# Kernel tuning notes

Hardware: AMD Instinct MI355X
Metric: run time of the kernel (lower is better)

The kernel has to match this reference:

```python
import jax, jax.numpy as jnp
import numpy as np

# Fixed multi-scale geometry implied by the module's hard-coded reshapes
# (48^2=2304, 24^2=576, 12^2=144; Len_q = 576).
SPATIAL = [(48, 48), (24, 24), (12, 12)]
NH, NP, NL = 6, 4, 3  # num_heads, num_points, num_levels


def _process_reference_points(rp):
    """rp: (B, 3024, 2) normalized refs over 3 levels -> (B, 576, 2).
    Mirrors the part1/part2/part3 averaging in MSDeformAttn.forward."""
    B = rp.shape[0]
    p1 = rp[:, :2304].reshape(B, 48, 48, 2).mean(axis=(1, 2))[:, None, :]
    p1 = jnp.broadcast_to(p1, (B, 576, 2))
    p2 = rp[:, 2304:2880].reshape(B, 576, 2)
    p3 = rp[:, 2880:].reshape(B, 12, 12, 2)
    p3 = jax.image.resize(p3, (B, 24, 24, 2), 'bilinear')  # align_corners=False
    p3 = p3.reshape(B, 576, 2)
    return (p1 + p2 + p3) / 3.0


def _bilinear_sample(val_l, coords, Hl, Wl):
    """val_l: (B, Hl*Wl, nh, d) one level's values.
    coords: (B, Lq, nh, P, 2) normalized (x, y) sampling locations.
    Returns (B, Lq, P, nh, d) bilinearly sampled values (zero padding)."""
    B, Lq, nh, P, _ = coords.shape
    px = coords[..., 0] * Wl - 0.5
    py = coords[..., 1] * Hl - 0.5
    x0 = jnp.floor(px)
    y0 = jnp.floor(py)
    lx = px - x0
    ly = py - y0
    x0i = x0.astype(jnp.int32)
    y0i = y0.astype(jnp.int32)

    def _flat(a):  # (B,Lq,nh,P) -> (B,Lq*P,nh,1) matching value layout
        return a.transpose(0, 1, 3, 2).reshape(B, Lq * P, nh, 1)

    def gather(xi, yi):
        valid = (xi >= 0) & (xi < Wl) & (yi >= 0) & (yi < Hl)
        xi_c = jnp.clip(xi, 0, Wl - 1)
        yi_c = jnp.clip(yi, 0, Hl - 1)
        idx = _flat(yi_c * Wl + xi_c)
        v = jnp.take_along_axis(val_l, idx, axis=1)  # (B,Lq*P,nh,d)
        return v * _flat(valid).astype(val_l.dtype)

    w00 = _flat((1 - lx) * (1 - ly))
    w10 = _flat(lx * (1 - ly))
    w01 = _flat((1 - lx) * ly)
    w11 = _flat(lx * ly)
    out = (gather(x0i, y0i) * w00 + gather(x0i + 1, y0i) * w10 +
           gather(x0i, y0i + 1) * w01 + gather(x0i + 1, y0i + 1) * w11)
    return out.reshape(B, Lq, P, nh, -1)


def setup_inputs() -> dict:
    key = jax.random.key(0)
    ks = jax.random.split(key, 8)
    B, C = 32, 384
    Lq, Lv = 576, 3024
    # reference points exactly as get_reference_points builds them
    refs = []
    for (Hl, Wl) in SPATIAL:
        ry, rx = np.meshgrid(np.linspace(0.5, Hl - 0.5, Hl) / Hl,
                             np.linspace(0.5, Wl - 0.5, Wl) / Wl, indexing='ij')
        refs.append(np.stack([rx.ravel(), ry.ravel()], -1))
    rp = np.concatenate(refs, 0).astype(np.float32)  # (3024, 2)
    rp = np.broadcast_to(rp[None, :, None, :], (B, Lv, 1, 2)).copy()
    s = 1.0 / np.sqrt(C)
    return {
        'query': jax.random.normal(ks[0], (B, Lq, C), jnp.float32),
        'value': jax.random.normal(ks[1], (B, Lv, C), jnp.float32),
        'reference_points': jnp.asarray(rp),
        'W_value': jax.random.normal(ks[2], (C, C), jnp.float32) * s,
        'b_value': jnp.zeros((C,), jnp.float32),
        'W_off': jax.random.normal(ks[3], (C, NH * NL * NP * 2), jnp.float32) * 0.01,
        'b_off': jnp.zeros((NH * NL * NP * 2,), jnp.float32),
        'W_attn': jax.random.normal(ks[4], (C, NH * NL * NP), jnp.float32) * s,
        'b_attn': jnp.zeros((NH * NL * NP,), jnp.float32),
        'W_out': jax.random.normal(ks[5], (C, C), jnp.float32) * s,
        'b_out': jnp.zeros((C,), jnp.float32),
    }


def reference(query, value, reference_points, W_value, b_value, W_off, b_off,
              W_attn, b_attn, W_out, b_out):
    B, Lq, C = query.shape
    d = C // NH
    val = (value @ W_value + b_value).reshape(B, -1, NH, d)
    off = (query @ W_off + b_off).reshape(B, Lq, NH, NL, NP, 2)
    attn = jax.nn.softmax((query @ W_attn + b_attn)
                          .reshape(B, Lq, NH, NL * NP), axis=-1)
    attn = attn.reshape(B, Lq, NH, NL, NP)
    ref = _process_reference_points(reference_points.reshape(B, -1, 2))
    coords = off + ref[:, :, None, None, None, :]  # (B,Lq,nh,L,P,2)
    out = jnp.zeros((B, Lq, NH, d), query.dtype)
    start = 0
    for l, (Hl, Wl) in enumerate(SPATIAL):
        val_l = val[:, start:start + Hl * Wl]
        sampled = _bilinear_sample(val_l, coords[:, :, :, l], Hl, Wl)
        out = out + jnp.einsum('bqpnd,bqnp->bqnd', sampled, attn[:, :, :, l])
        start += Hl * Wl
    return out.reshape(B, Lq, NH * d) @ W_out + b_out
```

## Files before the change

### kernel.cpp

```cpp
#include <hip/hip_runtime.h>
#include <cmath>

#define B_SZ   32
#define LQ     576
#define LV     3024
#define CDIM   384
#define NHEAD  6
#define DHEAD  64
#define NLVL   3
#define NPTS   4
#define NPROJ  216
#define NPROJP 256

typedef short    bx4 __attribute__((ext_vector_type(4)));
typedef short    bx8 __attribute__((ext_vector_type(8)));
typedef float    fx4 __attribute__((ext_vector_type(4)));
typedef _Float16 hx8 __attribute__((ext_vector_type(8)));

__device__ __forceinline__ short f2bf(float f) {
    unsigned u = __builtin_bit_cast(unsigned, f);
    unsigned r = (u + 0x7FFFu + ((u >> 16) & 1u)) >> 16;
    return (short)r;
}
__device__ __forceinline__ float bf2f(unsigned short u) {
    return __builtin_bit_cast(float, ((unsigned)u) << 16);
}
__device__ __forceinline__ short f2h(float f) {
    return __builtin_bit_cast(short, (_Float16)f);
}

__global__ __launch_bounds__(256) void cast_transpose_kernel(
    const float* __restrict__ W, short* __restrict__ Wt, int K, int N)
{
    int idx = blockIdx.x * 256 + threadIdx.x;
    if (idx >= K * N) return;
    int n = idx / K, k = idx - n * K;
    Wt[idx] = f2bf(W[(size_t)k * N + n]);
}

__global__ __launch_bounds__(256) void prep_proj_f16_kernel(
    const float* __restrict__ W_off, const float* __restrict__ b_off,
    const float* __restrict__ W_attn, const float* __restrict__ b_attn,
    short* __restrict__ Wf, float* __restrict__ bc)
{
    int idx = blockIdx.x * 256 + threadIdx.x;
    if (idx >= NPROJP * CDIM) return;
    int n = idx / CDIM, k = idx - n * CDIM;
    float w = 0.f;
    if (n < 144)           w = W_off[(size_t)k * 144 + n];
    else if (n < NPROJ)    w = W_attn[(size_t)k * 72 + (n - 144)];
    Wf[idx] = f2h(w);
    if (idx < NPROJP)
        bc[idx] = (idx < 144) ? b_off[idx]
                 : (idx < NPROJ ? b_attn[idx - 144] : 0.f);
}

template <int ATYPE, bool F16, bool OUT_BF16, bool NGUARD>
__global__ __launch_bounds__(256, 3) void gemm128_kernel(
    const void* __restrict__ Av, const short* __restrict__ Bt,
    const float* __restrict__ bias, void* __restrict__ Cout,
    int M, int K, int Nact, int ldc)
{
    __shared__ short As[128 * 72];
    __shared__ short Bs[128 * 72];

    const int tid = threadIdx.x;
    const int n0 = blockIdx.x * 128;
    const int m0 = blockIdx.y * 128;

    const int w  = tid >> 6;
    const int l  = tid & 63;
    const int wr = (w & 1) * 64;
    const int wc = (w >> 1) * 64;
    const int lr = l & 15;
    const int ko = (l >> 4) * 8;

    fx4 acc[4][4] = {};

    for (int k0 = 0; k0 < K; k0 += 64) {
        if (ATYPE == 1) {
            const short* A = (const short*)Av;
            #pragma unroll
            for (int r = 0; r < 4; ++r) {
                const int id = tid + r * 256;
                const int m  = id >> 3;
                const int k8 = (id & 7) << 3;
                *(bx8*)&As[m * 72 + k8] = *(const bx8*)(A + (size_t)(m0 + m) * K + k0 + k8);
            }
        } else {
            const float* A = (const float*)Av;
            #pragma unroll
            for (int r = 0; r < 8; ++r) {
                const int id = tid + r * 256;
                const int m  = id >> 4;
                const int kq = (id & 15) << 2;
                const float4 v = *(const float4*)(A + (size_t)(m0 + m) * K + k0 + kq);
                bx4 s;
                if (ATYPE == 0) {
                    s[0] = f2bf(v.x); s[1] = f2bf(v.y); s[2] = f2bf(v.z); s[3] = f2bf(v.w);
                } else {
                    s[0] = f2h(v.x);  s[1] = f2h(v.y);  s[2] = f2h(v.z);  s[3] = f2h(v.w);
                }
                *(bx4*)&As[m * 72 + kq] = s;
            }
        }
        #pragma unroll
        for (int r = 0; r < 4; ++r) {
            const int id = tid + r * 256;
            const int n  = id >> 3;
            const int k8 = (id & 7) << 3;
            *(bx8*)&Bs[n * 72 + k8] = *(const bx8*)(Bt + (size_t)(n0 + n) * K + k0 + k8);
        }
        __syncthreads();

        #pragma unroll
        for (int ks = 0; ks < 2; ++ks) {
            bx8 af[4], bf[4];
            #pragma unroll
            for (int i = 0; i < 4; ++i)
                af[i] = *(const bx8*)&As[(wr + i * 16 + lr) * 72 + ks * 32 + ko];
            #pragma unroll
            for (int j = 0; j < 4; ++j)
                bf[j] = *(const bx8*)&Bs[(wc + j * 16 + lr) * 72 + ks * 32 + ko];
            #pragma unroll
            for (int i = 0; i < 4; ++i)
                #pragma unroll
                for (int j = 0; j < 4; ++j) {
                    if (F16)
                        acc[i][j] = __builtin_amdgcn_mfma_f32_16x16x32_f16(
                            __builtin_bit_cast(hx8, af[i]),
                            __builtin_bit_cast(hx8, bf[j]), acc[i][j], 0, 0, 0);
                    else
                        acc[i][j] = __builtin_amdgcn_mfma_f32_16x16x32_bf16(
                            af[i], bf[j], acc[i][j], 0, 0, 0);
                }
        }
        __syncthreads();
    }

    const int rrow = (l >> 4) * 4;
    #pragma unroll
    for (int j = 0; j < 4; ++j) {
        const int col = n0 + wc + j * 16 + lr;
        if (NGUARD && col >= Nact) continue;
        const float bv = bias[col];
        #pragma unroll
        for (int i = 0; i < 4; ++i) {
            const int row = m0 + wr + i * 16 + rrow;
            #pragma unroll
            for (int r = 0; r < 4; ++r) {
                if (OUT_BF16)
                    ((short*)Cout)[(size_t)(row + r) * ldc + col] = f2bf(acc[i][j][r] + bv);
                else
                    ((float*)Cout)[(size_t)(row + r) * ldc + col] = acc[i][j][r] + bv;
            }
        }
    }
}

__global__ __launch_bounds__(256) void ref_kernel(
    const float* __restrict__ rp, float* __restrict__ refp)
{
    const int b = blockIdx.x;
    const float* r = rp + (size_t)b * LV * 2;
    const int tid = threadIdx.x;

    __shared__ float redx[256], redy[256];
    float sx = 0.f, sy = 0.f;
    for (int i = tid; i < 2304; i += 256) {
        sx += r[2 * i + 0];
        sy += r[2 * i + 1];
    }
    redx[tid] = sx; redy[tid] = sy;
    __syncthreads();
    for (int s = 128; s > 0; s >>= 1) {
        if (tid < s) { redx[tid] += redx[tid + s]; redy[tid] += redy[tid + s]; }
        __syncthreads();
    }
    const float p1x = redx[0] * (1.f / 2304.f);
    const float p1y = redy[0] * (1.f / 2304.f);

    const float* g = r + 2880 * 2;
    for (int q = tid; q < 576; q += 256) {
        const float p2x = r[(2304 + q) * 2 + 0];
        const float p2y = r[(2304 + q) * 2 + 1];
        const int qy = q / 24, qx = q % 24;
        const float syc = fminf(fmaxf(0.5f * qy - 0.25f, 0.f), 11.f);
        const float sxc = fminf(fmaxf(0.5f * qx - 0.25f, 0.f), 11.f);
        int y0 = min((int)syc, 10);
        int x0 = min((int)sxc, 10);
        const float fy = syc - (float)y0, fx = sxc - (float)x0;
        const float v00x = g[(y0 * 12 + x0) * 2 + 0],     v00y = g[(y0 * 12 + x0) * 2 + 1];
        const float v10x = g[(y0 * 12 + x0 + 1) * 2 + 0], v10y = g[(y0 * 12 + x0 + 1) * 2 + 1];
        const float v01x = g[((y0 + 1) * 12 + x0) * 2 + 0],     v01y = g[((y0 + 1) * 12 + x0) * 2 + 1];
        const float v11x = g[((y0 + 1) * 12 + x0 + 1) * 2 + 0], v11y = g[((y0 + 1) * 12 + x0 + 1) * 2 + 1];
        const float p3x = (1.f - fy) * ((1.f - fx) * v00x + fx * v10x)
                        + fy * ((1.f - fx) * v01x + fx * v11x);
        const float p3y = (1.f - fy) * ((1.f - fx) * v00y + fx * v10y)
                        + fy * ((1.f - fx) * v01y + fx * v11y);
        refp[((size_t)b * LQ + q) * 2 + 0] = (p1x + p2x + p3x) * (1.f / 3.f);
        refp[((size_t)b * LQ + q) * 2 + 1] = (p1y + p2y + p3y) * (1.f / 3.f);
    }
}

__global__ __launch_bounds__(192) void sample_kernel(
    const unsigned short* __restrict__ val, const float* __restrict__ proj,
    const float* __restrict__ refp, unsigned* __restrict__ mid)
{
    const int i = blockIdx.x;
    const int g = i & 7;
    const int r = i >> 3;
    const int b = g * 4 + (r / LQ);
    const int q = r - (r / LQ) * LQ;
    const int bq = b * LQ + q;
    const int tid = threadIdx.x;

    __shared__ float attn[72];
    __shared__ int   sloc[72][4];
    __shared__ float swt[72][4];

    if (tid < 72) {
        attn[tid] = proj[(size_t)bq * NPROJ + 144 + tid];

        const int h = tid / 12;
        const int rr = tid % 12;
        const int l = rr >> 2;
        const int p = rr & 3;

        const int HL[3] = {48, 24, 12};
        const int ST[3] = {0, 2304, 2880};
        const int Hl = HL[l], Wl = HL[l], st = ST[l];

        const float rx = refp[bq * 2 + 0];
        const float ry = refp[bq * 2 + 1];
        const int oc = ((h * NLVL + l) * NPTS + p) * 2;
        const float cx = proj[(size_t)bq * NPROJ + oc + 0] + rx;
        const float cy = proj[(size_t)bq * NPROJ + oc + 1] + ry;

        const float px = cx * (float)Wl - 0.5f;
        const float py = cy * (float)Hl - 0.5f;
        const float x0f = floorf(px), y0f = floorf(py);
        const float lx = px - x0f, ly = py - y0f;
        const int x0 = (int)x0f, y0 = (int)y0f;

        #pragma unroll
        for (int k = 0; k < 4; ++k) {
            const int dx = k & 1, dy = k >> 1;
            const int xi = x0 + dx, yi = y0 + dy;
            const bool v = (xi >= 0) && (xi < Wl) && (yi >= 0) && (yi < Hl);
            const int xc = min(max(xi, 0), Wl - 1);
            const int yc = min(max(yi, 0), Hl - 1);
            sloc[tid][k] = st + yc * Wl + xc;
            const float wx = dx ? lx : 1.f - lx;
            const float wy = dy ? ly : 1.f - ly;
            swt[tid][k] = v ? wx * wy : 0.f;
        }
    }
    __syncthreads();

    if (tid < NHEAD) {
        float mx = -1e30f;
        #pragma unroll
        for (int j = 0; j < 12; ++j) mx = fmaxf(mx, attn[tid * 12 + j]);
        float s = 0.f;
        #pragma unroll
        for (int j = 0; j < 12; ++j) {
            const float e = expf(attn[tid * 12 + j] - mx);
            attn[tid * 12 + j] = e;
            s += e;
        }
        const float inv = 1.f / s;
        #pragma unroll
        for (int j = 0; j < 12; ++j) attn[tid * 12 + j] *= inv;
    }
    __syncthreads();

    const int h  = tid >> 5;
    const int c2 = (tid & 31) << 1;
    const unsigned* vp = (const unsigned*)(val + (size_t)b * LV * CDIM + h * DHEAD + c2);
    float acc0 = 0.f, acc1 = 0.f;
    #pragma unroll
    for (int s = 0; s < 12; ++s) {
        const int j = h * 12 + s;
        const float a = attn[j];
        float s0 = 0.f, s1 = 0.f;
        #pragma unroll
        for (int k = 0; k < 4; ++k) {
            const unsigned u = vp[(size_t)sloc[j][k] * (CDIM / 2)];
            const float lo = __builtin_bit_cast(float, u << 16);
            const float hi = __builtin_bit_cast(float, u & 0xFFFF0000u);
            s0 += swt[j][k] * lo;
            s1 += swt[j][k] * hi;
        }
        acc0 += a * s0;
        acc1 += a * s1;
    }
    const unsigned lo = (unsigned)(unsigned short)f2bf(acc0);
    const unsigned hi = (unsigned)(unsigned short)f2bf(acc1);
    mid[((size_t)bq * CDIM + h * DHEAD + c2) >> 1] = lo | (hi << 16);
}

extern "C" void kernel_launch(void* const* d_in, const int* in_sizes, int n_in,
                              void* d_out, int out_size, void* d_ws, size_t ws_size,
                              hipStream_t stream)
{
    (void)in_sizes; (void)n_in; (void)out_size; (void)ws_size;

    const float* query   = (const float*)d_in[0];
    const float* value   = (const float*)d_in[1];
    const float* rp      = (const float*)d_in[2];
    const float* W_value = (const float*)d_in[3];
    const float* b_value = (const float*)d_in[4];
    const float* W_off   = (const float*)d_in[5];
    const float* b_off   = (const float*)d_in[6];
    const float* W_attn  = (const float*)d_in[7];
    const float* b_attn  = (const float*)d_in[8];
    const float* W_out   = (const float*)d_in[9];
    const float* b_out   = (const float*)d_in[10];
    float* out = (float*)d_out;

    char* p = (char*)d_ws;
    auto take = [&](size_t bytes) { char* q = p; p += (bytes + 255) & ~(size_t)255; return q; };
    short* val  = (short*)take((size_t)B_SZ * LV * CDIM * 2);
    short* mid  = (short*)take((size_t)B_SZ * LQ * CDIM * 2);
    short* Wtv  = (short*)take((size_t)CDIM * CDIM * 2);
    short* Wto  = (short*)take((size_t)CDIM * CDIM * 2);
    short* Wf   = (short*)take((size_t)NPROJP * CDIM * 2);
    float* proj = (float*)take((size_t)B_SZ * LQ * NPROJ * 4);
    float* refp = (float*)take((size_t)B_SZ * LQ * 2 * 4);
    float* bc   = (float*)take((size_t)NPROJP * 4);

    const int Mv = B_SZ * LV;
    const int Mq = B_SZ * LQ;

    cast_transpose_kernel<<<(CDIM * CDIM + 255) / 256, 256, 0, stream>>>(
        W_value, Wtv, CDIM, CDIM);
    cast_transpose_kernel<<<(CDIM * CDIM + 255) / 256, 256, 0, stream>>>(
        W_out, Wto, CDIM, CDIM);
    prep_proj_f16_kernel<<<(NPROJP * CDIM + 255) / 256, 256, 0, stream>>>(
        W_off, b_off, W_attn, b_attn, Wf, bc);

    gemm128_kernel<0, false, true, false><<<dim3(3, Mv / 128), 256, 0, stream>>>(
        value, Wtv, b_value, val, Mv, CDIM, CDIM, CDIM);
    gemm128_kernel<2, true, false, true><<<dim3(2, Mq / 128), 256, 0, stream>>>(
        query, Wf, bc, proj, Mq, CDIM, NPROJ, NPROJ);
    ref_kernel<<<B_SZ, 256, 0, stream>>>(rp, refp);
    sample_kernel<<<Mq, 192, 0, stream>>>(
        (const unsigned short*)val, proj, refp, (unsigned*)mid);
    gemm128_kernel<1, false, false, false><<<dim3(3, Mq / 128), 256, 0, stream>>>(
        mid, Wto, b_out, out, Mq, CDIM, CDIM, CDIM);
}
```

Measured before the change: 426.8 us.

## Use direct global-to-LDS loads with swizzled layout for bf16 GEMMs

Adds a separate fp32-to-bf16 cast pass for the value tensor. The value and output projections then use a GEMM kernel that loads tiles directly into LDS via global_load_lds with an XOR swizzle instead of padding. This is meant to cut register staging and LDS bank conflicts in the GEMM main loop. In exchange, the value tensor now makes an extra full round trip through memory for the cast, and a new workspace buffer is needed.

```diff
diff --git a/kernel.cpp b/kernel.cpp
--- a/kernel.cpp
+++ b/kernel.cpp
@@ -29,6 +29,18 @@
     return __builtin_bit_cast(short, (_Float16)f);
 }
 
+__global__ __launch_bounds__(256) void cast_bf16_kernel(
+    const float4* __restrict__ in, bx8* __restrict__ outv, int n8)
+{
+    const int i = blockIdx.x * 256 + threadIdx.x;
+    if (i >= n8) return;
+    const float4 a = in[2 * i], b = in[2 * i + 1];
+    bx8 s;
+    s[0] = f2bf(a.x); s[1] = f2bf(a.y); s[2] = f2bf(a.z); s[3] = f2bf(a.w);
+    s[4] = f2bf(b.x); s[5] = f2bf(b.y); s[6] = f2bf(b.z); s[7] = f2bf(b.w);
+    outv[i] = s;
+}
+
 __global__ __launch_bounds__(256) void cast_transpose_kernel(
     const float* __restrict__ W, short* __restrict__ Wt, int K, int N)
 {
@@ -55,11 +67,94 @@
                  : (idx < NPROJ ? b_attn[idx - 144] : 0.f);
 }
 
-template <int ATYPE, bool F16, bool OUT_BF16, bool NGUARD>
-__global__ __launch_bounds__(256, 3) void gemm128_kernel(
-    const void* __restrict__ Av, const short* __restrict__ Bt,
+template <bool OUT_BF16>
+__global__ __launch_bounds__(256) void gemm_dma_kernel(
+    const short* __restrict__ A, const short* __restrict__ Bt,
     const float* __restrict__ bias, void* __restrict__ Cout,
-    int M, int K, int Nact, int ldc)
+    int M, int K)
+{
+    constexpr int N = 384;
+    __shared__ short As[128 * 64];
+    __shared__ short Bs[128 * 64];
+
+    const int tid = threadIdx.x;
+    const int n0 = blockIdx.x * 128;
+    const int m0 = blockIdx.y * 128;
+
+    const int w  = tid >> 6;
+    const int l  = tid & 63;
+    const int wr = (w & 1) * 64;
+    const int wc = (w >> 1) * 64;
+    const int lr = l & 15;
+    const int q  = l >> 4;
+
+    const int rg  = l >> 3;
+    const int cg  = l & 7;
+    const int csw = cg ^ rg;
+
+    fx4 acc[4][4] = {};
+
+    for (int k0 = 0; k0 < K; k0 += 64) {
+        #pragma unroll
+        for (int t = 0; t < 4; ++t) {
+            const int rbase = w * 32 + t * 8;
+            const short* gA = A + (size_t)(m0 + rbase + rg) * K + k0 + csw * 8;
+            __builtin_amdgcn_global_load_lds(
+                (const __attribute__((address_space(1))) void*)gA,
+                (__attribute__((address_space(3))) void*)&As[rbase * 64],
+                16, 0, 0);
+            const short* gB = Bt + (size_t)(n0 + rbase + rg) * K + k0 + csw * 8;
+            __builtin_amdgcn_global_load_lds(
+                (const __attribute__((address_space(1))) void*)gB,
+                (__attribute__((address_space(3))) void*)&Bs[rbase * 64],
+                16, 0, 0);
+        }
+        __syncthreads();
+
+        #pragma unroll
+        for (int ks = 0; ks < 2; ++ks) {
+            bx8 af[4], bf[4];
+            #pragma unroll
+            for (int i = 0; i < 4; ++i)
+                af[i] = *(const bx8*)&As[(wr + i * 16 + lr) * 64 +
+                                         (((ks * 4 + q) ^ (lr & 7)) << 3)];
+            #pragma unroll
+            for (int j = 0; j < 4; ++j)
+                bf[j] = *(const bx8*)&Bs[(wc + j * 16 + lr) * 64 +
+                                         (((ks * 4 + q) ^ (lr & 7)) << 3)];
+            #pragma unroll
+            for (int i = 0; i < 4; ++i)
+                #pragma unroll
+                for (int j = 0; j < 4; ++j)
+                    acc[i][j] = __builtin_amdgcn_mfma_f32_16x16x32_bf16(
+                        af[i], bf[j], acc[i][j], 0, 0, 0);
+        }
+        __syncthreads();
+    }
+
+    const int rrow = q * 4;
+    #pragma unroll
+    for (int j = 0; j < 4; ++j) {
+        const int col = n0 + wc + j * 16 + lr;
+        const float bv = bias[col];
+        #pragma unroll
+        for (int i = 0; i < 4; ++i) {
+            const int row = m0 + wr + i * 16 + rrow;
+            #pragma unroll
+            for (int r = 0; r < 4; ++r) {
+                if (OUT_BF16)
+                    ((short*)Cout)[(size_t)(row + r) * N + col] = f2bf(acc[i][j][r] + bv);
+                else
+                    ((float*)Cout)[(size_t)(row + r) * N + col] = acc[i][j][r] + bv;
+            }
+        }
+    }
+}
+
+__global__ __launch_bounds__(256) void gemm_proj_kernel(
+    const float* __restrict__ A, const short* __restrict__ Wf,
+    const float* __restrict__ bias, float* __restrict__ C,
+    int M, int K)
 {
     __shared__ short As[128 * 72];
     __shared__ short Bs[128 * 72];
@@ -78,38 +173,22 @@
     fx4 acc[4][4] = {};
 
     for (int k0 = 0; k0 < K; k0 += 64) {
-        if (ATYPE == 1) {
-            const short* A = (const short*)Av;
-            #pragma unroll
-            for (int r = 0; r < 4; ++r) {
-                const int id = tid + r * 256;
-                const int m  = id >> 3;
-                const int k8 = (id & 7) << 3;
-                *(bx8*)&As[m * 72 + k8] = *(const bx8*)(A + (size_t)(m0 + m) * K + k0 + k8);
-            }
-        } else {
-            const float* A = (const float*)Av;
-            #pragma unroll
-            for (int r = 0; r < 8; ++r) {
-                const int id = tid + r * 256;
-                const int m  = id >> 4;
-                const int kq = (id & 15) << 2;
-                const float4 v = *(const float4*)(A + (size_t)(m0 + m) * K + k0 + kq);
-                bx4 s;
-                if (ATYPE == 0) {
-                    s[0] = f2bf(v.x); s[1] = f2bf(v.y); s[2] = f2bf(v.z); s[3] = f2bf(v.w);
-                } else {
-                    s[0] = f2h(v.x);  s[1] = f2h(v.y);  s[2] = f2h(v.z);  s[3] = f2h(v.w);
-                }
-                *(bx4*)&As[m * 72 + kq] = s;
-            }
+        #pragma unroll
+        for (int r = 0; r < 8; ++r) {
+            const int id = tid + r * 256;
+            const int m  = id >> 4;
+            const int kq = (id & 15) << 2;
+            const float4 v = *(const float4*)(A + (size_t)(m0 + m) * K + k0 + kq);
+            bx4 s;
+            s[0] = f2h(v.x); s[1] = f2h(v.y); s[2] = f2h(v.z); s[3] = f2h(v.w);
+            *(bx4*)&As[m * 72 + kq] = s;
         }
         #pragma unroll
         for (int r = 0; r < 4; ++r) {
             const int id = tid + r * 256;
             const int n  = id >> 3;
             const int k8 = (id & 7) << 3;
-            *(bx8*)&Bs[n * 72 + k8] = *(const bx8*)(Bt + (size_t)(n0 + n) * K + k0 + k8);
+            *(bx8*)&Bs[n * 72 + k8] = *(const bx8*)(Wf + (size_t)(n0 + n) * K + k0 + k8);
         }
         __syncthreads();
 
@@ -125,15 +204,10 @@
             #pragma unroll
             for (int i = 0; i < 4; ++i)
                 #pragma unroll
-                for (int j = 0; j < 4; ++j) {
-                    if (F16)
-                        acc[i][j] = __builtin_amdgcn_mfma_f32_16x16x32_f16(
-                            __builtin_bit_cast(hx8, af[i]),
-                            __builtin_bit_cast(hx8, bf[j]), acc[i][j], 0, 0, 0);
-                    else
-                        acc[i][j] = __builtin_amdgcn_mfma_f32_16x16x32_bf16(
-                            af[i], bf[j], acc[i][j], 0, 0, 0);
-                }
+                for (int j = 0; j < 4; ++j)
+                    acc[i][j] = __builtin_amdgcn_mfma_f32_16x16x32_f16(
+                        __builtin_bit_cast(hx8, af[i]),
+                        __builtin_bit_cast(hx8, bf[j]), acc[i][j], 0, 0, 0);
         }
         __syncthreads();
     }
@@ -142,18 +216,14 @@
     #pragma unroll
     for (int j = 0; j < 4; ++j) {
         const int col = n0 + wc + j * 16 + lr;
-        if (NGUARD && col >= Nact) continue;
+        if (col >= NPROJ) continue;
         const float bv = bias[col];
         #pragma unroll
         for (int i = 0; i < 4; ++i) {
             const int row = m0 + wr + i * 16 + rrow;
             #pragma unroll
-            for (int r = 0; r < 4; ++r) {
-                if (OUT_BF16)
-                    ((short*)Cout)[(size_t)(row + r) * ldc + col] = f2bf(acc[i][j][r] + bv);
-                else
-                    ((float*)Cout)[(size_t)(row + r) * ldc + col] = acc[i][j][r] + bv;
-            }
+            for (int r = 0; r < 4; ++r)
+                C[(size_t)(row + r) * NPROJ + col] = acc[i][j][r] + bv;
         }
     }
 }
@@ -321,6 +391,7 @@
 
     char* p = (char*)d_ws;
     auto take = [&](size_t bytes) { char* q = p; p += (bytes + 255) & ~(size_t)255; return q; };
+    short* valb = (short*)take((size_t)B_SZ * LV * CDIM * 2);
     short* val  = (short*)take((size_t)B_SZ * LV * CDIM * 2);
     short* mid  = (short*)take((size_t)B_SZ * LQ * CDIM * 2);
     short* Wtv  = (short*)take((size_t)CDIM * CDIM * 2);
@@ -332,6 +403,7 @@
 
     const int Mv = B_SZ * LV;
     const int Mq = B_SZ * LQ;
+    const int nv8 = Mv * CDIM / 8;
 
     cast_transpose_kernel<<<(CDIM * CDIM + 255) / 256, 256, 0, stream>>>(
         W_value, Wtv, CDIM, CDIM);
@@ -339,14 +411,16 @@
         W_out, Wto, CDIM, CDIM);
     prep_proj_f16_kernel<<<(NPROJP * CDIM + 255) / 256, 256, 0, stream>>>(
         W_off, b_off, W_attn, b_attn, Wf, bc);
-
-    gemm128_kernel<0, false, true, false><<<dim3(3, Mv / 128), 256, 0, stream>>>(
-        value, Wtv, b_value, val, Mv, CDIM, CDIM, CDIM);
-    gemm128_kernel<2, true, false, true><<<dim3(2, Mq / 128), 256, 0, stream>>>(
-        query, Wf, bc, proj, Mq, CDIM, NPROJ, NPROJ);
+    cast_bf16_kernel<<<(nv8 + 255) / 256, 256, 0, stream>>>(
+        (const float4*)value, (bx8*)valb, nv8);
+
+    gemm_dma_kernel<true><<<dim3(3, Mv / 128), 256, 0, stream>>>(
+        valb, Wtv, b_value, val, Mv, CDIM);
+    gemm_proj_kernel<<<dim3(2, Mq / 128), 256, 0, stream>>>(
+        query, Wf, bc, proj, Mq, CDIM);
     ref_kernel<<<B_SZ, 256, 0, stream>>>(rp, refp);
     sample_kernel<<<Mq, 192, 0, stream>>>(
         (const unsigned short*)val, proj, refp, (unsigned*)mid);
-    gemm128_kernel<1, false, false, false><<<dim3(3, Mq / 128), 256, 0, stream>>>(
-        mid, Wto, b_out, out, Mq, CDIM, CDIM, CDIM);
-}
+    gemm_dma_kernel<false><<<dim3(3, Mq / 128), 256, 0, stream>>>(
+        mid, Wto, b_out, out, Mq, CDIM);
+}
```

Result: faster. 399.1 us (-6.5%).
